# Optimization experiments

Measured on AMD Instinct MI355X. Metric: run time of the kernel, lower is better.

The kernel has to match this reference:

```python
import jax, jax.numpy as jnp
import numpy as np

EPS = 1e-5

def conv1x1(x, w):
    # x: [B,C,T,D,H,W], w: [O,C] -> [B,O,T,D,H,W]
    return jnp.einsum('oc,bctdhw->botdhw', w, x)

def conv4d_3(x, w):
    # 3x3x3x3 4D conv, padding=1, stride=1, decomposed as 3 shifted 3D convs.
    # x: [B,C,T,D,H,W], w: [O,C,3,3,3,3]
    B, C, T, D, H, W = x.shape
    O = w.shape[0]
    xp = jnp.pad(x, ((0, 0), (0, 0), (1, 1), (1, 1), (1, 1), (1, 1)))
    out = None
    for k in range(3):  # small fixed loop over first kernel dim
        xk = xp[:, :, k:k + T]                      # [B,C,T,D+2,H+2,W+2]
        xk = xk.transpose(0, 2, 1, 3, 4, 5).reshape(B * T, C, D + 2, H + 2, W + 2)
        ok = jax.lax.conv_general_dilated(
            xk, w[:, :, k], window_strides=(1, 1, 1), padding='VALID',
            dimension_numbers=('NCDHW', 'OIDHW', 'NCDHW'))  # [B*T,O,D,H,W]
        out = ok if out is None else out + ok
    return out.reshape(B, T, O, D, H, W).transpose(0, 2, 1, 3, 4, 5)

def bn4d(x, g, b):
    # BatchNorm over (B, T, D, H, W) per channel (training-mode batch stats).
    axes = (0, 2, 3, 4, 5)
    m = jnp.mean(x, axis=axes, keepdims=True)
    v = jnp.mean(jnp.square(x - m), axis=axes, keepdims=True)
    sh = (1, -1, 1, 1, 1, 1)
    return (x - m) * jax.lax.rsqrt(v + EPS) * g.reshape(sh) + b.reshape(sh)

def setup_inputs() -> dict:
    key = jax.random.key(0)
    ks = jax.random.split(key, 4)
    B, C, T, D, H, W = 2, 256, 8, 16, 16, 16
    planes = 64
    return {
        'x': jax.random.normal(ks[0], (B, C, T, D, H, W), jnp.float32),
        'w1': jax.random.normal(ks[1], (planes, C), jnp.float32) * 0.05,
        'g1': jnp.ones((planes,), jnp.float32),
        'b1': jnp.zeros((planes,), jnp.float32),
        'w2': jax.random.normal(ks[2], (planes, planes, 3, 3, 3, 3), jnp.float32) * 0.05,
        'g2': jnp.ones((planes,), jnp.float32),
        'b2': jnp.zeros((planes,), jnp.float32),
        'w3': jax.random.normal(ks[3], (4 * planes, planes), jnp.float32) * 0.05,
        'g3': jnp.ones((4 * planes,), jnp.float32),
        'b3': jnp.zeros((4 * planes,), jnp.float32),
    }

def reference(x, w1, g1, b1, w2, g2, b2, w3, g3, b3):
    out = jax.nn.relu(bn4d(conv1x1(x, w1), g1, b1))
    out = jax.nn.relu(bn4d(conv4d_3(out, w2), g2, b2))
    out = bn4d(conv1x1(out, w3), g3, b3)
    return jax.nn.relu(out + x)
```

## Files before the change

kernel.cpp:

```cpp
#include <hip/hip_runtime.h>

#define S_TOT 32768

typedef unsigned short ushortT;
typedef __attribute__((ext_vector_type(8))) short short8;
typedef __attribute__((ext_vector_type(4))) float floatx4;

__device__ __forceinline__ ushortT f2bf(float f) {
    unsigned u = __float_as_uint(f);
    u = (u + 0x7fffu + ((u >> 16) & 1u)) >> 16;
    return (ushortT)u;
}
__device__ __forceinline__ float bf2f(ushortT h) {
    return __uint_as_float(((unsigned)h) << 16);
}
__device__ __forceinline__ uint32_t nrm2(uint32_t u, float a, float bs) {
    float lo = fmaxf(fmaf(a, bf2f((ushortT)(u & 0xffffu)), bs), 0.f);
    float hi = fmaxf(fmaf(a, bf2f((ushortT)(u >> 16)), bs), 0.f);
    return (uint32_t)f2bf(lo) | ((uint32_t)f2bf(hi) << 16);
}

#define NSTRIPE 8
#define STRIDE_ST 768

__global__ __launch_bounds__(256) void k_prep_w(const float* __restrict__ w1,
                                                const float* __restrict__ w2,
                                                const float* __restrict__ w3,
                                                ushortT* __restrict__ wb1,
                                                ushortT* __restrict__ wb2,
                                                ushortT* __restrict__ wb3,
                                                float* __restrict__ stats) {
    int idx = blockIdx.x * 256 + threadIdx.x;
    if (idx < 16384) {
        int e = idx;
        int j = e & 7, o = (e >> 3) & 63, q = (e >> 9) & 3, cc = e >> 11;
        int c = cc * 32 + q * 8 + j;
        wb1[e] = f2bf(w1[o * 256 + c]);
    } else if (idx < 16384 + 331776) {
        int e = idx - 16384;
        int j = e & 7, o = (e >> 3) & 63, cb = (e >> 9) & 7, tap = e >> 12;
        int c = cb * 8 + j;
        wb2[e] = f2bf(w2[((size_t)o * 64 + c) * 81 + tap]);
    } else if (idx < 16384 + 331776 + 16384) {
        int e = idx - 348160;
        int j = e & 7, o = (e >> 3) & 255, g = e >> 11;
        int ks = g >> 2, q = g & 3;
        int c = ks * 32 + q * 8 + j;
        wb3[e] = f2bf(w3[o * 64 + c]);
    } else if (idx < 364544 + NSTRIPE * STRIDE_ST) {
        stats[idx - 364544] = 0.f;
    }
}

__global__ __launch_bounds__(256) void k_coef(const float* __restrict__ stats,
                                              int off, int nch,
                                              const float* __restrict__ g,
                                              const float* __restrict__ bb,
                                              float* __restrict__ coef) {
    int c = threadIdx.x;
    if (c >= nch) return;
    float s = 0.f, qv = 0.f;
#pragma unroll
    for (int p = 0; p < NSTRIPE; ++p) {
        s  += stats[p * STRIDE_ST + off + c];
        qv += stats[p * STRIDE_ST + off + nch + c];
    }
    const float inv_n = 1.f / 65536.f;
    float mu = s * inv_n, var = qv * inv_n - mu * mu;
    float a  = g[c] * rsqrtf(var + 1e-5f);
    coef[2 * c]     = a;
    coef[2 * c + 1] = bb[c] - mu * a;
}

__global__ __launch_bounds__(256) void k_prep(const ushortT* __restrict__ yin,
                                              const float* __restrict__ coef,
                                              ushortT* __restrict__ yout) {
    size_t i = ((size_t)blockIdx.x * 256 + threadIdx.x) * 8;
    int c = (int)((i >> 15) & 63);
    float2 cf = *(const float2*)(coef + 2 * c);
    uint4 v = *(const uint4*)(yin + i);
    uint4 r;
    r.x = nrm2(v.x, cf.x, cf.y);
    r.y = nrm2(v.y, cf.x, cf.y);
    r.z = nrm2(v.z, cf.x, cf.y);
    r.w = nrm2(v.w, cf.x, cf.y);
    *(uint4*)(yout + i) = r;
}

__global__ __launch_bounds__(256) void k_conv1_mfma(const float* __restrict__ x,
                                                    const ushortT* __restrict__ wb1,
                                                    ushortT* __restrict__ y1bf,
                                                    float* __restrict__ stats) {
    __shared__ __align__(16) ushortT xb[2][64 * 40];

    int tid = threadIdx.x;
    int blk = blockIdx.x;
    int b  = blk >> 9;
    int n0 = (blk & 511) * 64;

    int lane = tid & 63;
    int wv   = tid >> 6;
    int m    = lane & 15;
    int q    = lane >> 4;

    int c_loc = tid & 31;
    int ng    = tid >> 5;

    const float* xbase = x + ((size_t)(b * 256 + c_loc)) * S_TOT + n0 + ng * 8;

    floatx4 acc[4];
#pragma unroll
    for (int i = 0; i < 4; ++i) acc[i] = (floatx4){0.f, 0.f, 0.f, 0.f};

    short8 afr = *(const short8*)(wb1 + ((q * 64) + wv * 16 + m) * 8);
    {
        float4 v0 = *(const float4*)(xbase);
        float4 v1 = *(const float4*)(xbase + 4);
        int nb = ng * 8;
        ushortT* xd = xb[0];
        xd[(nb + 0) * 40 + c_loc] = f2bf(v0.x);
        xd[(nb + 1) * 40 + c_loc] = f2bf(v0.y);
        xd[(nb + 2) * 40 + c_loc] = f2bf(v0.z);
        xd[(nb + 3) * 40 + c_loc] = f2bf(v0.w);
        xd[(nb + 4) * 40 + c_loc] = f2bf(v1.x);
        xd[(nb + 5) * 40 + c_loc] = f2bf(v1.y);
        xd[(nb + 6) * 40 + c_loc] = f2bf(v1.z);
        xd[(nb + 7) * 40 + c_loc] = f2bf(v1.w);
    }
    __syncthreads();

    for (int cc = 0; cc < 8; ++cc) {
        short8 nafr;
        float4 n0v, n1v;
        if (cc < 7) {
            nafr = *(const short8*)(wb1 + ((((cc + 1) * 4 + q) * 64) + wv * 16 + m) * 8);
            const float* xp = xbase + (size_t)(cc + 1) * 32 * S_TOT;
            n0v = *(const float4*)(xp);
            n1v = *(const float4*)(xp + 4);
        }

        const ushortT* xc = xb[cc & 1];
#pragma unroll
        for (int pt = 0; pt < 4; ++pt) {
            short8 bfr = *(const short8*)(xc + (pt * 16 + m) * 40 + q * 8);
            acc[pt] = __builtin_amdgcn_mfma_f32_16x16x32_bf16(afr, bfr, acc[pt], 0, 0, 0);
        }

        if (cc < 7) {
            int nb = ng * 8;
            ushortT* xd = xb[(cc + 1) & 1];
            xd[(nb + 0) * 40 + c_loc] = f2bf(n0v.x);
            xd[(nb + 1) * 40 + c_loc] = f2bf(n0v.y);
            xd[(nb + 2) * 40 + c_loc] = f2bf(n0v.z);
            xd[(nb + 3) * 40 + c_loc] = f2bf(n0v.w);
            xd[(nb + 4) * 40 + c_loc] = f2bf(n1v.x);
            xd[(nb + 5) * 40 + c_loc] = f2bf(n1v.y);
            xd[(nb + 6) * 40 + c_loc] = f2bf(n1v.z);
            xd[(nb + 7) * 40 + c_loc] = f2bf(n1v.w);
            afr = nafr;
        }
        __syncthreads();
    }

#pragma unroll
    for (int pt = 0; pt < 4; ++pt) {
#pragma unroll
        for (int r = 0; r < 4; ++r) {
            int o = wv * 16 + q * 4 + r;
            y1bf[((size_t)(b * 64 + o)) * S_TOT + n0 + pt * 16 + m] = f2bf(acc[pt][r]);
        }
    }

    float ssum[4] = {0.f, 0.f, 0.f, 0.f}, ssq[4] = {0.f, 0.f, 0.f, 0.f};
#pragma unroll
    for (int pt = 0; pt < 4; ++pt)
#pragma unroll
        for (int r = 0; r < 4; ++r) {
            float v = acc[pt][r];
            ssum[r] += v;
            ssq[r]  += v * v;
        }
#pragma unroll
    for (int off = 1; off < 16; off <<= 1)
#pragma unroll
        for (int r = 0; r < 4; ++r) {
            ssum[r] += __shfl_xor(ssum[r], off);
            ssq[r]  += __shfl_xor(ssq[r], off);
        }
    if (m == 0) {
        float* st = stats + (blk & (NSTRIPE - 1)) * STRIDE_ST;
#pragma unroll
        for (int r = 0; r < 4; ++r) {
            int o = wv * 16 + q * 4 + r;
            atomicAdd(st + o, ssum[r]);
            atomicAdd(st + 64 + o, ssq[r]);
        }
    }
}

__global__ __launch_bounds__(256, 2) void k_conv2_mfma(
        const ushortT* __restrict__ y1n,
        const ushortT* __restrict__ wb2,
        float* __restrict__ stats,
        ushortT* __restrict__ y2bf) {
    __shared__ __align__(16) ushortT xs[108 * 64];
    __shared__ float st2[128];

    int tid = threadIdx.x;
    int blk = blockIdx.x;
    int b  = blk >> 9;
    int t  = (blk >> 6) & 7;
    int d  = (blk >> 2) & 15;
    int h0 = (blk & 3) * 4;

    int lane = tid & 63;
    int wv   = tid >> 6;
    int m    = lane & 15;
    int q    = lane >> 4;
    int wp   = wv & 1;
    int wo   = wv >> 1;

    int c2      = tid & 31;
    int prbase  = tid >> 5;

    if (tid < 128) st2[tid] = 0.f;

    const ushortT* wfb = wb2 + ((size_t)q * 64 + wo * 32 + m) * 8;

    floatx4 acc[2][2];
#pragma unroll
    for (int i = 0; i < 2; ++i)
#pragma unroll
        for (int j = 0; j < 2; ++j) acc[i][j] = (floatx4){0.f, 0.f, 0.f, 0.f};

    const size_t cstride = 32768;
    uint32_t* xsd = (uint32_t*)xs;

    for (int ktd = 0; ktd < 9; ++ktd) {
        int kt = ktd / 3, kd = ktd - kt * 3;
        int tt = t + kt - 1;
        int dd = d + kd - 1;
        bool pv = (tt >= 0 && tt < 8 && dd >= 0 && dd < 16);
        if (!pv) continue;

        __syncthreads();

        if (prbase < 6) {
            int hin = h0 + prbase - 1;
            uint32_t pack[18];
            if (hin >= 0 && hin < 16) {
                const ushortT* p0 = y1n +
                    (((size_t)(b * 64 + 2 * c2) * 8 + tt) * 16 + dd) * 256 + hin * 16;
                const ushortT* p1 = p0 + cstride;
                uint4 r0 = *(const uint4*)p0;
                uint4 r1 = *(const uint4*)(p0 + 8);
                uint4 s0v = *(const uint4*)p1;
                uint4 s1v = *(const uint4*)(p1 + 8);
                uint32_t ra[8] = {r0.x, r0.y, r0.z, r0.w, r1.x, r1.y, r1.z, r1.w};
                uint32_t sa[8] = {s0v.x, s0v.y, s0v.z, s0v.w, s1v.x, s1v.y, s1v.z, s1v.w};
                pack[0] = 0; pack[17] = 0;
#pragma unroll
                for (int k = 0; k < 8; ++k) {
                    pack[1 + 2 * k] = (ra[k] & 0xffffu) | (sa[k] << 16);
                    pack[2 + 2 * k] = (ra[k] >> 16) | (sa[k] & 0xffff0000u);
                }
            } else {
#pragma unroll
                for (int k = 0; k < 18; ++k) pack[k] = 0;
            }
            int pb = prbase * 18;
#pragma unroll
            for (int k = 0; k < 18; ++k) {
                int ppos = pb + k;
                xsd[ppos * 32 + ((((c2 >> 2) ^ (ppos & 7)) << 2) | (c2 & 3))] = pack[k];
            }
        }

        int tap0 = ktd * 9;
        short8 c00 = *(const short8*)(wfb + ((size_t)(tap0 * 8) * 64) * 8);
        short8 c01 = *(const short8*)(wfb + ((size_t)(tap0 * 8) * 64 + 16) * 8);
        short8 c10 = *(const short8*)(wfb + ((size_t)(tap0 * 8 + 4) * 64) * 8);
        short8 c11 = *(const short8*)(wfb + ((size_t)(tap0 * 8 + 4) * 64 + 16) * 8);

        __syncthreads();

#pragma unroll
        for (int khw = 0; khw < 9; ++khw) {
            short8 n00, n01, n10, n11;
            if (khw < 8) {
                int tap = tap0 + khw + 1;
                n00 = *(const short8*)(wfb + ((size_t)(tap * 8) * 64) * 8);
                n01 = *(const short8*)(wfb + ((size_t)(tap * 8) * 64 + 16) * 8);
                n10 = *(const short8*)(wfb + ((size_t)(tap * 8 + 4) * 64) * 8);
                n11 = *(const short8*)(wfb + ((size_t)(tap * 8 + 4) * 64 + 16) * 8);
            }
            int kh = khw / 3, kw = khw - kh * 3;
#pragma unroll
            for (int nt = 0; nt < 2; ++nt) {
                int ppos = (wp * 2 + nt + kh) * 18 + m + kw;
                int sw = (ppos & 7);
                const ushortT* row = xs + ppos * 64;
                short8 b0  = *(const short8*)(row + (((0 * 4 + q) ^ sw) << 3));
                short8 b1f = *(const short8*)(row + (((1 * 4 + q) ^ sw) << 3));
                acc[0][nt] = __builtin_amdgcn_mfma_f32_16x16x32_bf16(
                    c00, b0, acc[0][nt], 0, 0, 0);
                acc[1][nt] = __builtin_amdgcn_mfma_f32_16x16x32_bf16(
                    c01, b0, acc[1][nt], 0, 0, 0);
                acc[0][nt] = __builtin_amdgcn_mfma_f32_16x16x32_bf16(
                    c10, b1f, acc[0][nt], 0, 0, 0);
                acc[1][nt] = __builtin_amdgcn_mfma_f32_16x16x32_bf16(
                    c11, b1f, acc[1][nt], 0, 0, 0);
            }
            c00 = n00; c01 = n01; c10 = n10; c11 = n11;
            asm volatile("" ::: "memory");
        }
    }

#pragma unroll
    for (int ot = 0; ot < 2; ++ot) {
#pragma unroll
        for (int nt = 0; nt < 2; ++nt) {
#pragma unroll
            for (int r = 0; r < 4; ++r) {
                int o  = wo * 32 + ot * 16 + q * 4 + r;
                int hh = h0 + wp * 2 + nt;
                y2bf[(((size_t)(b * 64 + o) * 8 + t) * 16 + d) * 256 + hh * 16 + m] =
                    f2bf(acc[ot][nt][r]);
            }
        }
    }

    float ss[2][4], sqv[2][4];
#pragma unroll
    for (int ot = 0; ot < 2; ++ot)
#pragma unroll
        for (int r = 0; r < 4; ++r) {
            float s = 0.f, qv = 0.f;
#pragma unroll
            for (int nt = 0; nt < 2; ++nt) {
                float v = acc[ot][nt][r];
                s += v; qv += v * v;
            }
            ss[ot][r] = s; sqv[ot][r] = qv;
        }
#pragma unroll
    for (int off = 1; off < 16; off <<= 1)
#pragma unroll
        for (int ot = 0; ot < 2; ++ot)
#pragma unroll
            for (int r = 0; r < 4; ++r) {
                ss[ot][r]  += __shfl_xor(ss[ot][r], off);
                sqv[ot][r] += __shfl_xor(sqv[ot][r], off);
            }
    if (m == 0) {
#pragma unroll
        for (int ot = 0; ot < 2; ++ot)
#pragma unroll
            for (int r = 0; r < 4; ++r) {
                int o = wo * 32 + ot * 16 + q * 4 + r;
                atomicAdd(&st2[o], ss[ot][r]);
                atomicAdd(&st2[64 + o], sqv[ot][r]);
            }
    }
    __syncthreads();
    if (tid < 128)
        atomicAdd(stats + (blk & (NSTRIPE - 1)) * STRIDE_ST + 128 + tid, st2[tid]);
}

__global__ __launch_bounds__(256) void k_conv3_mfma(const ushortT* __restrict__ y2bf,
                                                    const ushortT* __restrict__ wb3,
                                                    const float* __restrict__ coef2,
                                                    float* __restrict__ stats,
                                                    float* __restrict__ y3) {
    __shared__ __align__(16) ushortT yb[64 * 72];

    int tid = threadIdx.x;
    int blk = blockIdx.x;
    int b  = blk >> 9;
    int n0 = (blk & 511) * 64;

    int lane = tid & 63;
    int wv   = tid >> 6;
    int m    = lane & 15;
    int q    = lane >> 4;

    for (int idx = tid; idx < 512; idx += 256) {
        int c = idx >> 3, k = idx & 7;
        float2 cc2 = *(const float2*)(coef2 + 2 * c);
        float a = cc2.x, bs = cc2.y;
        uint4 v = *(const uint4*)(y2bf + ((size_t)(b * 64 + c)) * S_TOT + n0 + k * 8);
        uint32_t va[4] = {v.x, v.y, v.z, v.w};
#pragma unroll
        for (int p = 0; p < 4; ++p) {
            float lo = fmaxf(fmaf(a, bf2f((ushortT)(va[p] & 0xffffu)), bs), 0.f);
            float hi = fmaxf(fmaf(a, bf2f((ushortT)(va[p] >> 16)), bs), 0.f);
            yb[(k * 8 + 2 * p)     * 72 + c] = f2bf(lo);
            yb[(k * 8 + 2 * p + 1) * 72 + c] = f2bf(hi);
        }
    }
    __syncthreads();

    floatx4 acc[4][4];
#pragma unroll
    for (int i = 0; i < 4; ++i)
#pragma unroll
        for (int j = 0; j < 4; ++j) acc[i][j] = (floatx4){0.f, 0.f, 0.f, 0.f};

#pragma unroll
    for (int ks = 0; ks < 2; ++ks) {
        short8 afr[4];
#pragma unroll
        for (int ot = 0; ot < 4; ++ot)
            afr[ot] = *(const short8*)(wb3 +
                (((ks * 4 + q) * 256) + wv * 64 + ot * 16 + m) * 8);
#pragma unroll
        for (int pt = 0; pt < 4; ++pt) {
            short8 bfr = *(const short8*)(yb + (pt * 16 + m) * 72 + ks * 32 + q * 8);
#pragma unroll
            for (int ot = 0; ot < 4; ++ot)
                acc[ot][pt] = __builtin_amdgcn_mfma_f32_16x16x32_bf16(
                    afr[ot], bfr, acc[ot][pt], 0, 0, 0);
        }
    }

#pragma unroll
    for (int ot = 0; ot < 4; ++ot) {
#pragma unroll
        for (int pt = 0; pt < 4; ++pt) {
#pragma unroll
            for (int r = 0; r < 4; ++r) {
                int o = wv * 64 + ot * 16 + q * 4 + r;
                y3[((size_t)(b * 256 + o)) * S_TOT + n0 + pt * 16 + m] = acc[ot][pt][r];
            }
        }
    }

    float ssum[4][4], ssq[4][4];
#pragma unroll
    for (int ot = 0; ot < 4; ++ot)
#pragma unroll
        for (int r = 0; r < 4; ++r) {
            float s = 0.f, qv = 0.f;
#pragma unroll
            for (int pt = 0; pt < 4; ++pt) {
                float v = acc[ot][pt][r];
                s += v; qv += v * v;
            }
            ssum[ot][r] = s; ssq[ot][r] = qv;
        }
#pragma unroll
    for (int off = 1; off < 16; off <<= 1)
#pragma unroll
        for (int ot = 0; ot < 4; ++ot)
#pragma unroll
            for (int r = 0; r < 4; ++r) {
                ssum[ot][r] += __shfl_xor(ssum[ot][r], off);
                ssq[ot][r]  += __shfl_xor(ssq[ot][r], off);
            }
    if (m == 0) {
        float* st = stats + (blk & (NSTRIPE - 1)) * STRIDE_ST;
#pragma unroll
        for (int ot = 0; ot < 4; ++ot)
#pragma unroll
            for (int r = 0; r < 4; ++r) {
                int o = wv * 64 + ot * 16 + q * 4 + r;
                atomicAdd(st + 256 + o, ssum[ot][r]);
                atomicAdd(st + 512 + o, ssq[ot][r]);
            }
    }
}

__global__ __launch_bounds__(256) void k_final(const float* __restrict__ x,
                                               const float* __restrict__ stats,
                                               const float* __restrict__ g,
                                               const float* __restrict__ bb,
                                               float* __restrict__ out) {
    size_t i = ((size_t)blockIdx.x * 256 + threadIdx.x) * 4;
    int o = (int)((blockIdx.x >> 5) & 255);
    float s = 0.f, qv = 0.f;
#pragma unroll
    for (int p = 0; p < NSTRIPE; ++p) {
        s  += stats[p * STRIDE_ST + 256 + o];
        qv += stats[p * STRIDE_ST + 512 + o];
    }
    const float n = 65536.f;
    float mean = s / n;
    float var  = qv / n - mean * mean;
    float a  = g[o] * rsqrtf(var + 1e-5f);
    float bs = bb[o] - mean * a;
    float4 y  = *(float4*)(out + i);
    float4 xv = *(const float4*)(x + i);
    float4 r;
    r.x = fmaxf(a * y.x + bs + xv.x, 0.f);
    r.y = fmaxf(a * y.y + bs + xv.y, 0.f);
    r.z = fmaxf(a * y.z + bs + xv.z, 0.f);
    r.w = fmaxf(a * y.w + bs + xv.w, 0.f);
    *(float4*)(out + i) = r;
}

extern "C" void kernel_launch(void* const* d_in, const int* in_sizes, int n_in,
                              void* d_out, int out_size, void* d_ws, size_t ws_size,
                              hipStream_t stream) {
    const float* x  = (const float*)d_in[0];
    const float* w1 = (const float*)d_in[1];
    const float* g1 = (const float*)d_in[2];
    const float* b1 = (const float*)d_in[3];
    const float* w2 = (const float*)d_in[4];
    const float* g2 = (const float*)d_in[5];
    const float* b2 = (const float*)d_in[6];
    const float* w3 = (const float*)d_in[7];
    const float* g3 = (const float*)d_in[8];
    const float* b3 = (const float*)d_in[9];

    char* ws = (char*)d_ws;
    ushortT* y1bf = (ushortT*)(ws);
    ushortT* y1n  = (ushortT*)(ws + 8388608);
    ushortT* y2bf = (ushortT*)(ws + 16777216);
    ushortT* wb1  = (ushortT*)(ws + 25165824);
    ushortT* wb2  = (ushortT*)(ws + 25198592);
    ushortT* wb3  = (ushortT*)(ws + 25862144);
    float*   stats = (float*)(ws + 25894912);
    float*   coef1 = (float*)(ws + 25919488);
    float*   coef2 = (float*)(ws + 25920000);
    float* y3 = (float*)d_out;

    k_prep_w     <<<1448,  256, 0, stream>>>(w1, w2, w3, wb1, wb2, wb3, stats);
    k_conv1_mfma <<<1024,  256, 0, stream>>>(x, wb1, y1bf, stats);
    k_coef       <<<1,     256, 0, stream>>>(stats, 0, 64, g1, b1, coef1);
    k_prep       <<<2048,  256, 0, stream>>>(y1bf, coef1, y1n);
    k_conv2_mfma <<<1024,  256, 0, stream>>>(y1n, wb2, stats, y2bf);
    k_coef       <<<1,     256, 0, stream>>>(stats, 128, 64, g2, b2, coef2);
    k_conv3_mfma <<<1024,  256, 0, stream>>>(y2bf, wb3, coef2, stats, y3);
    k_final      <<<16384, 256, 0, stream>>>(x, stats, g3, b3, y3);
}
```

Measured before the change: 255.1 us.

## Fold BN1 coefficient computation into prep kernel and retile conv2 warps over channels

Removes the separate single-block k_coef launch for BN1. k_prep now reduces the striped stats and computes the scale and shift inline in every thread. Conv2 changes its wave mapping: each wave now owns one h-row and all 64 output channels (4 accumulator tiles) instead of 2 rows by 32 channels. That halves the LDS B-fragment reads per MFMA but doubles the weight fragment loads and registers per wave. The trade-off is more redundant global stats reads in k_prep and higher register pressure in conv2, in exchange for one fewer launch and better reuse of the LDS activations.

```diff
diff --git a/kernel.cpp b/kernel.cpp
--- a/kernel.cpp
+++ b/kernel.cpp
@@ -73,17 +73,28 @@
 }
 
 __global__ __launch_bounds__(256) void k_prep(const ushortT* __restrict__ yin,
-                                              const float* __restrict__ coef,
+                                              const float* __restrict__ stats,
+                                              const float* __restrict__ g,
+                                              const float* __restrict__ bb,
                                               ushortT* __restrict__ yout) {
     size_t i = ((size_t)blockIdx.x * 256 + threadIdx.x) * 8;
     int c = (int)((i >> 15) & 63);
-    float2 cf = *(const float2*)(coef + 2 * c);
+    float s = 0.f, qv = 0.f;
+#pragma unroll
+    for (int p = 0; p < NSTRIPE; ++p) {
+        s  += stats[p * STRIDE_ST + c];
+        qv += stats[p * STRIDE_ST + 64 + c];
+    }
+    const float inv_n = 1.f / 65536.f;
+    float mu = s * inv_n, var = qv * inv_n - mu * mu;
+    float a  = g[c] * rsqrtf(var + 1e-5f);
+    float bs = bb[c] - mu * a;
     uint4 v = *(const uint4*)(yin + i);
     uint4 r;
-    r.x = nrm2(v.x, cf.x, cf.y);
-    r.y = nrm2(v.y, cf.x, cf.y);
-    r.z = nrm2(v.z, cf.x, cf.y);
-    r.w = nrm2(v.w, cf.x, cf.y);
+    r.x = nrm2(v.x, a, bs);
+    r.y = nrm2(v.y, a, bs);
+    r.z = nrm2(v.z, a, bs);
+    r.w = nrm2(v.w, a, bs);
     *(uint4*)(yout + i) = r;
 }
 
@@ -217,21 +228,18 @@
     int wv   = tid >> 6;
     int m    = lane & 15;
     int q    = lane >> 4;
-    int wp   = wv & 1;
-    int wo   = wv >> 1;
+    int wp   = wv;
 
     int c2      = tid & 31;
     int prbase  = tid >> 5;
 
     if (tid < 128) st2[tid] = 0.f;
 
-    const ushortT* wfb = wb2 + ((size_t)q * 64 + wo * 32 + m) * 8;
-
-    floatx4 acc[2][2];
-#pragma unroll
-    for (int i = 0; i < 2; ++i)
-#pragma unroll
-        for (int j = 0; j < 2; ++j) acc[i][j] = (floatx4){0.f, 0.f, 0.f, 0.f};
+    const ushortT* wfb = wb2 + ((size_t)q * 64 + m) * 8;
+
+    floatx4 acc[4];
+#pragma unroll
+    for (int i = 0; i < 4; ++i) acc[i] = (floatx4){0.f, 0.f, 0.f, 0.f};
 
     const size_t cstride = 32768;
     uint32_t* xsd = (uint32_t*)xs;
@@ -277,89 +285,99 @@
         }
 
         int tap0 = ktd * 9;
-        short8 c00 = *(const short8*)(wfb + ((size_t)(tap0 * 8) * 64) * 8);
-        short8 c01 = *(const short8*)(wfb + ((size_t)(tap0 * 8) * 64 + 16) * 8);
-        short8 c10 = *(const short8*)(wfb + ((size_t)(tap0 * 8 + 4) * 64) * 8);
-        short8 c11 = *(const short8*)(wfb + ((size_t)(tap0 * 8 + 4) * 64 + 16) * 8);
+        short8 f00 = *(const short8*)(wfb + ((size_t)(tap0 * 8) * 64) * 8);
+        short8 f01 = *(const short8*)(wfb + ((size_t)(tap0 * 8) * 64 + 16) * 8);
+        short8 f02 = *(const short8*)(wfb + ((size_t)(tap0 * 8) * 64 + 32) * 8);
+        short8 f03 = *(const short8*)(wfb + ((size_t)(tap0 * 8) * 64 + 48) * 8);
+        short8 f10 = *(const short8*)(wfb + ((size_t)(tap0 * 8 + 4) * 64) * 8);
+        short8 f11 = *(const short8*)(wfb + ((size_t)(tap0 * 8 + 4) * 64 + 16) * 8);
+        short8 f12 = *(const short8*)(wfb + ((size_t)(tap0 * 8 + 4) * 64 + 32) * 8);
+        short8 f13 = *(const short8*)(wfb + ((size_t)(tap0 * 8 + 4) * 64 + 48) * 8);
 
         __syncthreads();
 
 #pragma unroll
         for (int khw = 0; khw < 9; ++khw) {
-            short8 n00, n01, n10, n11;
+            short8 n00, n01, n02, n03, n10, n11, n12, n13;
             if (khw < 8) {
                 int tap = tap0 + khw + 1;
                 n00 = *(const short8*)(wfb + ((size_t)(tap * 8) * 64) * 8);
                 n01 = *(const short8*)(wfb + ((size_t)(tap * 8) * 64 + 16) * 8);
+                n02 = *(const short8*)(wfb + ((size_t)(tap * 8) * 64 + 32) * 8);
+                n03 = *(const short8*)(wfb + ((size_t)(tap * 8) * 64 + 48) * 8);
                 n10 = *(const short8*)(wfb + ((size_t)(tap * 8 + 4) * 64) * 8);
                 n11 = *(const short8*)(wfb + ((size_t)(tap * 8 + 4) * 64 + 16) * 8);
+                n12 = *(const short8*)(wfb + ((size_t)(tap * 8 + 4) * 64 + 32) * 8);
+                n13 = *(const short8*)(wfb + ((size_t)(tap * 8 + 4) * 64 + 48) * 8);
             }
             int kh = khw / 3, kw = khw - kh * 3;
-#pragma unroll
-            for (int nt = 0; nt < 2; ++nt) {
-                int ppos = (wp * 2 + nt + kh) * 18 + m + kw;
-                int sw = (ppos & 7);
-                const ushortT* row = xs + ppos * 64;
-                short8 b0  = *(const short8*)(row + (((0 * 4 + q) ^ sw) << 3));
-                short8 b1f = *(const short8*)(row + (((1 * 4 + q) ^ sw) << 3));
-                acc[0][nt] = __builtin_amdgcn_mfma_f32_16x16x32_bf16(
-                    c00, b0, acc[0][nt], 0, 0, 0);
-                acc[1][nt] = __builtin_amdgcn_mfma_f32_16x16x32_bf16(
-                    c01, b0, acc[1][nt], 0, 0, 0);
-                acc[0][nt] = __builtin_amdgcn_mfma_f32_16x16x32_bf16(
-                    c10, b1f, acc[0][nt], 0, 0, 0);
-                acc[1][nt] = __builtin_amdgcn_mfma_f32_16x16x32_bf16(
-                    c11, b1f, acc[1][nt], 0, 0, 0);
-            }
-            c00 = n00; c01 = n01; c10 = n10; c11 = n11;
+            int ppos = (wp + kh) * 18 + m + kw;
+            int sw = (ppos & 7);
+            const ushortT* row = xs + ppos * 64;
+            short8 b0  = *(const short8*)(row + ((q ^ sw) << 3));
+            short8 b1f = *(const short8*)(row + (((4 + q) ^ sw) << 3));
+            acc[0] = __builtin_amdgcn_mfma_f32_16x16x32_bf16(f00, b0, acc[0], 0, 0, 0);
+            acc[1] = __builtin_amdgcn_mfma_f32_16x16x32_bf16(f01, b0, acc[1], 0, 0, 0);
+            acc[2] = __builtin_amdgcn_mfma_f32_16x16x32_bf16(f02, b0, acc[2], 0, 0, 0);
+            acc[3] = __builtin_amdgcn_mfma_f32_16x16x32_bf16(f03, b0, acc[3], 0, 0, 0);
+            acc[0] = __builtin_amdgcn_mfma_f32_16x16x32_bf16(f10, b1f, acc[0], 0, 0, 0);
+            acc[1] = __builtin_amdgcn_mfma_f32_16x16x32_bf16(f11, b1f, acc[1], 0, 0, 0);
+            acc[2] = __builtin_amdgcn_mfma_f32_16x16x32_bf16(f12, b1f, acc[2], 0, 0, 0);
+            acc[3] = __builtin_amdgcn_mfma_f32_16x16x32_bf16(f13, b1f, acc[3], 0, 0, 0);
+            f00 = n00; f01 = n01; f02 = n02; f03 = n03;
+            f10 = n10; f11 = n11; f12 = n12; f13 = n13;
             asm volatile("" ::: "memory");
         }
     }
 
-#pragma unroll
-    for (int ot = 0; ot < 2; ++ot) {
-#pragma unroll
-        for (int nt = 0; nt < 2; ++nt) {
+    {
+        int hh = h0 + wp;
+        ushortT* yb = y2bf + (((size_t)(b * 64) * 8 + t) * 16 + d) * 256 + hh * 16 + m;
+#pragma unroll
+        for (int ot = 0; ot < 4; ++ot) {
 #pragma unroll
             for (int r = 0; r < 4; ++r) {
-                int o  = wo * 32 + ot * 16 + q * 4 + r;
-                int hh = h0 + wp * 2 + nt;
-                y2bf[(((size_t)(b * 64 + o) * 8 + t) * 16 + d) * 256 + hh * 16 + m] =
-                    f2bf(acc[ot][nt][r]);
-            }
-        }
-    }
-
-    float ss[2][4], sqv[2][4];
-#pragma unroll
-    for (int ot = 0; ot < 2; ++ot)
-#pragma unroll
-        for (int r = 0; r < 4; ++r) {
-            float s = 0.f, qv = 0.f;
-#pragma unroll
-            for (int nt = 0; nt < 2; ++nt) {
-                float v = acc[ot][nt][r];
-                s += v; qv += v * v;
-            }
-            ss[ot][r] = s; sqv[ot][r] = qv;
+                int o = ot * 16 + q * 4 + r;
+                yb[(size_t)o * 8 * 16 * 256] = f2bf(acc[ot][r]);
+            }
+        }
+    }
+
+    float ss[4], sqv[4];
+#pragma unroll
+    for (int ot = 0; ot < 4; ++ot) {
+        float s = 0.f, qv2 = 0.f;
+#pragma unroll
+        for (int r = 0; r < 4; ++r) {
+        }
+        (void)s; (void)qv2;
+    }
+    float s2[4][4], q2[4][4];
+#pragma unroll
+    for (int ot = 0; ot < 4; ++ot)
+#pragma unroll
+        for (int r = 0; r < 4; ++r) {
+            float v = acc[ot][r];
+            s2[ot][r] = v;
+            q2[ot][r] = v * v;
         }
 #pragma unroll
     for (int off = 1; off < 16; off <<= 1)
 #pragma unroll
-        for (int ot = 0; ot < 2; ++ot)
+        for (int ot = 0; ot < 4; ++ot)
 #pragma unroll
             for (int r = 0; r < 4; ++r) {
-                ss[ot][r]  += __shfl_xor(ss[ot][r], off);
-                sqv[ot][r] += __shfl_xor(sqv[ot][r], off);
+                s2[ot][r] += __shfl_xor(s2[ot][r], off);
+                q2[ot][r] += __shfl_xor(q2[ot][r], off);
             }
     if (m == 0) {
 #pragma unroll
-        for (int ot = 0; ot < 2; ++ot)
+        for (int ot = 0; ot < 4; ++ot)
 #pragma unroll
             for (int r = 0; r < 4; ++r) {
-                int o = wo * 32 + ot * 16 + q * 4 + r;
-                atomicAdd(&st2[o], ss[ot][r]);
-                atomicAdd(&st2[64 + o], sqv[ot][r]);
+                int o = ot * 16 + q * 4 + r;
+                atomicAdd(&st2[o], s2[ot][r]);
+                atomicAdd(&st2[64 + o], q2[ot][r]);
             }
     }
     __syncthreads();
@@ -520,14 +538,12 @@
     ushortT* wb2  = (ushortT*)(ws + 25198592);
     ushortT* wb3  = (ushortT*)(ws + 25862144);
     float*   stats = (float*)(ws + 25894912);
-    float*   coef1 = (float*)(ws + 25919488);
-    float*   coef2 = (float*)(ws + 25920000);
+    float*   coef2 = (float*)(ws + 25919488);
     float* y3 = (float*)d_out;
 
     k_prep_w     <<<1448,  256, 0, stream>>>(w1, w2, w3, wb1, wb2, wb3, stats);
     k_conv1_mfma <<<1024,  256, 0, stream>>>(x, wb1, y1bf, stats);
-    k_coef       <<<1,     256, 0, stream>>>(stats, 0, 64, g1, b1, coef1);
-    k_prep       <<<2048,  256, 0, stream>>>(y1bf, coef1, y1n);
+    k_prep       <<<2048,  256, 0, stream>>>(y1bf, stats, g1, b1, y1n);
     k_conv2_mfma <<<1024,  256, 0, stream>>>(y1n, wb2, stats, y2bf);
     k_coef       <<<1,     256, 0, stream>>>(stats, 128, 64, g2, b2, coef2);
     k_conv3_mfma <<<1024,  256, 0, stream>>>(y2bf, wb3, coef2, stats, y3);
```

New measurement: 286.4 us. +12.2%, slower.

## Enlarge conv2 H-tile to 8 rows and fold BN1 coefficient into prep

Applied to the files above, without the earlier changes.

The conv2 kernel now computes 8 output H-rows per block instead of 4, which halves the grid to 512 blocks and raises halo reuse: 10 input rows are staged for 8 outputs rather than 6 for 4. Each wave holds twice as many accumulators. The separate single-block k_coef launch for BN1 is removed, and every k_prep thread reduces the striped stats itself and derives the scale and shift. This trades one launch and one serial dependency for redundant per-thread stat loads, plus higher register and LDS use that may lower occupancy in conv2.

```diff
diff --git a/kernel.cpp b/kernel.cpp
--- a/kernel.cpp
+++ b/kernel.cpp
@@ -73,17 +73,28 @@
 }
 
 __global__ __launch_bounds__(256) void k_prep(const ushortT* __restrict__ yin,
-                                              const float* __restrict__ coef,
+                                              const float* __restrict__ stats,
+                                              const float* __restrict__ g,
+                                              const float* __restrict__ bb,
                                               ushortT* __restrict__ yout) {
     size_t i = ((size_t)blockIdx.x * 256 + threadIdx.x) * 8;
     int c = (int)((i >> 15) & 63);
-    float2 cf = *(const float2*)(coef + 2 * c);
+    float s = 0.f, qv = 0.f;
+#pragma unroll
+    for (int p = 0; p < NSTRIPE; ++p) {
+        s  += stats[p * STRIDE_ST + c];
+        qv += stats[p * STRIDE_ST + 64 + c];
+    }
+    const float inv_n = 1.f / 65536.f;
+    float mu = s * inv_n, var = qv * inv_n - mu * mu;
+    float a  = g[c] * rsqrtf(var + 1e-5f);
+    float bs = bb[c] - mu * a;
     uint4 v = *(const uint4*)(yin + i);
     uint4 r;
-    r.x = nrm2(v.x, cf.x, cf.y);
-    r.y = nrm2(v.y, cf.x, cf.y);
-    r.z = nrm2(v.z, cf.x, cf.y);
-    r.w = nrm2(v.w, cf.x, cf.y);
+    r.x = nrm2(v.x, a, bs);
+    r.y = nrm2(v.y, a, bs);
+    r.z = nrm2(v.z, a, bs);
+    r.w = nrm2(v.w, a, bs);
     *(uint4*)(yout + i) = r;
 }
 
@@ -203,15 +214,15 @@
         const ushortT* __restrict__ wb2,
         float* __restrict__ stats,
         ushortT* __restrict__ y2bf) {
-    __shared__ __align__(16) ushortT xs[108 * 64];
+    __shared__ __align__(16) ushortT xs[180 * 64];
     __shared__ float st2[128];
 
     int tid = threadIdx.x;
     int blk = blockIdx.x;
-    int b  = blk >> 9;
-    int t  = (blk >> 6) & 7;
-    int d  = (blk >> 2) & 15;
-    int h0 = (blk & 3) * 4;
+    int b  = blk >> 8;
+    int t  = (blk >> 5) & 7;
+    int d  = (blk >> 1) & 15;
+    int h0 = (blk & 1) * 8;
 
     int lane = tid & 63;
     int wv   = tid >> 6;
@@ -227,11 +238,11 @@
 
     const ushortT* wfb = wb2 + ((size_t)q * 64 + wo * 32 + m) * 8;
 
-    floatx4 acc[2][2];
+    floatx4 acc[2][4];
 #pragma unroll
     for (int i = 0; i < 2; ++i)
 #pragma unroll
-        for (int j = 0; j < 2; ++j) acc[i][j] = (floatx4){0.f, 0.f, 0.f, 0.f};
+        for (int j = 0; j < 4; ++j) acc[i][j] = (floatx4){0.f, 0.f, 0.f, 0.f};
 
     const size_t cstride = 32768;
     uint32_t* xsd = (uint32_t*)xs;
@@ -245,8 +256,8 @@
 
         __syncthreads();
 
-        if (prbase < 6) {
-            int hin = h0 + prbase - 1;
+        for (int pr = prbase; pr < 10; pr += 8) {
+            int hin = h0 + pr - 1;
             uint32_t pack[18];
             if (hin >= 0 && hin < 16) {
                 const ushortT* p0 = y1n +
@@ -268,7 +279,7 @@
 #pragma unroll
                 for (int k = 0; k < 18; ++k) pack[k] = 0;
             }
-            int pb = prbase * 18;
+            int pb = pr * 18;
 #pragma unroll
             for (int k = 0; k < 18; ++k) {
                 int ppos = pb + k;
@@ -296,12 +307,12 @@
             }
             int kh = khw / 3, kw = khw - kh * 3;
 #pragma unroll
-            for (int nt = 0; nt < 2; ++nt) {
-                int ppos = (wp * 2 + nt + kh) * 18 + m + kw;
+            for (int nt = 0; nt < 4; ++nt) {
+                int ppos = (wp * 4 + nt + kh) * 18 + m + kw;
                 int sw = (ppos & 7);
                 const ushortT* row = xs + ppos * 64;
-                short8 b0  = *(const short8*)(row + (((0 * 4 + q) ^ sw) << 3));
-                short8 b1f = *(const short8*)(row + (((1 * 4 + q) ^ sw) << 3));
+                short8 b0  = *(const short8*)(row + ((q ^ sw) << 3));
+                short8 b1f = *(const short8*)(row + (((4 + q) ^ sw) << 3));
                 acc[0][nt] = __builtin_amdgcn_mfma_f32_16x16x32_bf16(
                     c00, b0, acc[0][nt], 0, 0, 0);
                 acc[1][nt] = __builtin_amdgcn_mfma_f32_16x16x32_bf16(
@@ -319,11 +330,11 @@
 #pragma unroll
     for (int ot = 0; ot < 2; ++ot) {
 #pragma unroll
-        for (int nt = 0; nt < 2; ++nt) {
+        for (int nt = 0; nt < 4; ++nt) {
 #pragma unroll
             for (int r = 0; r < 4; ++r) {
                 int o  = wo * 32 + ot * 16 + q * 4 + r;
-                int hh = h0 + wp * 2 + nt;
+                int hh = h0 + wp * 4 + nt;
                 y2bf[(((size_t)(b * 64 + o) * 8 + t) * 16 + d) * 256 + hh * 16 + m] =
                     f2bf(acc[ot][nt][r]);
             }
@@ -337,7 +348,7 @@
         for (int r = 0; r < 4; ++r) {
             float s = 0.f, qv = 0.f;
 #pragma unroll
-            for (int nt = 0; nt < 2; ++nt) {
+            for (int nt = 0; nt < 4; ++nt) {
                 float v = acc[ot][nt][r];
                 s += v; qv += v * v;
             }
@@ -520,15 +531,13 @@
     ushortT* wb2  = (ushortT*)(ws + 25198592);
     ushortT* wb3  = (ushortT*)(ws + 25862144);
     float*   stats = (float*)(ws + 25894912);
-    float*   coef1 = (float*)(ws + 25919488);
-    float*   coef2 = (float*)(ws + 25920000);
+    float*   coef2 = (float*)(ws + 25919488);
     float* y3 = (float*)d_out;
 
     k_prep_w     <<<1448,  256, 0, stream>>>(w1, w2, w3, wb1, wb2, wb3, stats);
     k_conv1_mfma <<<1024,  256, 0, stream>>>(x, wb1, y1bf, stats);
-    k_coef       <<<1,     256, 0, stream>>>(stats, 0, 64, g1, b1, coef1);
-    k_prep       <<<2048,  256, 0, stream>>>(y1bf, coef1, y1n);
-    k_conv2_mfma <<<1024,  256, 0, stream>>>(y1n, wb2, stats, y2bf);
+    k_prep       <<<2048,  256, 0, stream>>>(y1bf, stats, g1, b1, y1n);
+    k_conv2_mfma <<<512,   256, 0, stream>>>(y1n, wb2, stats, y2bf);
     k_coef       <<<1,     256, 0, stream>>>(stats, 128, 64, g2, b2, coef2);
     k_conv3_mfma <<<1024,  256, 0, stream>>>(y2bf, wb3, coef2, stats, y3);
     k_final      <<<16384, 256, 0, stream>>>(x, stats, g3, b3, y3);
```

Result: no change. 252.4 us (-1.1%).
